# Optimization experiments

Measured on AMD Instinct MI355X. Metric: run time of the kernel, lower is better.

Reference implementation:

```python
import math
import jax, jax.numpy as jnp
import numpy as np

EMBED = 1024
HIDDEN = 1024
HEADS = 16


def setup_inputs() -> dict:
    key = jax.random.key(0)
    ks = jax.random.split(key, 9)
    B, S = 1, 4096
    s = 1.0 / math.sqrt(EMBED)
    return {
        "x": jax.random.normal(ks[0], (B, S, EMBED), dtype=jnp.float32),
        "Wq": jax.random.normal(ks[1], (EMBED, HIDDEN), dtype=jnp.float32) * s,
        "bq": jnp.zeros((HIDDEN,), dtype=jnp.float32),
        "Wk": jax.random.normal(ks[2], (EMBED, HIDDEN), dtype=jnp.float32) * s,
        "bk": jnp.zeros((HIDDEN,), dtype=jnp.float32),
        "Wv": jax.random.normal(ks[3], (EMBED, HIDDEN), dtype=jnp.float32) * s,
        "bv": jnp.zeros((HIDDEN,), dtype=jnp.float32),
        "Wo": jax.random.normal(ks[4], (EMBED, HIDDEN), dtype=jnp.float32) * s,
        "bo": jnp.zeros((HIDDEN,), dtype=jnp.float32),
    }


def reference(x, Wq, bq, Wk, bk, Wv, bv, Wo, bo):
    B, S, _ = x.shape
    Hd = HIDDEN // HEADS
    # projections: [B,S,hidden] -> [B,H,S,hd]
    def split_heads(t):
        return t.reshape(B, S, HEADS, Hd).transpose(0, 2, 1, 3)
    q = split_heads(x @ Wq + bq)
    k = split_heads(x @ Wk + bk)
    v = split_heads(x @ Wv + bv)
    scale = 1.0 / math.sqrt(EMBED / HEADS)
    scores = jnp.einsum("bhqd,bhkd->bhqk", q, k) * scale  # [B,H,S,S]
    attn = jax.nn.softmax(scores, axis=-1)
    ctx = jnp.einsum("bhqk,bhkd->bhqd", attn, v)
    ctx = ctx.transpose(0, 2, 1, 3).reshape(B, S, HIDDEN)
    return ctx @ Wo + bo
```

## Files before the change

### kernel.cpp

```cpp
#include <hip/hip_runtime.h>
#include <hip/hip_bf16.h>
#include <math.h>

typedef __bf16 bf16;
typedef bf16  bf16x2 __attribute__((ext_vector_type(2)));
typedef bf16  bf16x4 __attribute__((ext_vector_type(4)));
typedef bf16  bf16x8 __attribute__((ext_vector_type(8)));
typedef float f32x4  __attribute__((ext_vector_type(4)));
typedef float f32x16 __attribute__((ext_vector_type(16)));
typedef unsigned uint4v __attribute__((ext_vector_type(4)));

#define MFMA16(a, b, c) __builtin_amdgcn_mfma_f32_16x16x32_bf16((a), (b), (c), 0, 0, 0)
#define MFMA32(a, b, c) __builtin_amdgcn_mfma_f32_32x32x16_bf16((a), (b), (c), 0, 0, 0)

static constexpr int S  = 4096;
static constexpr int E  = 1024;
static constexpr int NH = 16;
static constexpr int HD = 64;

__device__ __forceinline__ void gload16(const bf16* g, bf16* l) {
    __builtin_amdgcn_global_load_lds(
        (const __attribute__((address_space(1))) void*)g,
        (__attribute__((address_space(3))) void*)l, 16, 0, 0);
}

__global__ void convert_f32_bf16(const float* __restrict__ in, bf16* __restrict__ out, int n) {
    int i = (blockIdx.x * blockDim.x + threadIdx.x) * 8;
    if (i < n) {
        float4 v0 = *(const float4*)(in + i);
        float4 v1 = *(const float4*)(in + i + 4);
        bf16x8 o = { (bf16)v0.x, (bf16)v0.y, (bf16)v0.z, (bf16)v0.w,
                     (bf16)v1.x, (bf16)v1.y, (bf16)v1.z, (bf16)v1.w };
        *(bf16x8*)(out + i) = o;
    }
}

__global__ void transpose_w(const float* __restrict__ W0, const float* __restrict__ W1,
                            const float* __restrict__ W2, const float* __restrict__ W3,
                            bf16* __restrict__ T0, bf16* __restrict__ T1,
                            bf16* __restrict__ T2, bf16* __restrict__ T3) {
    const float* W; bf16* T;
    switch (blockIdx.z) {
        case 0: W = W0; T = T0; break;
        case 1: W = W1; T = T1; break;
        case 2: W = W2; T = T2; break;
        default: W = W3; T = T3; break;
    }
    __shared__ float tile[64][65];
    int k0 = blockIdx.x * 64, n0 = blockIdx.y * 64;
    #pragma unroll
    for (int i = 0; i < 16; i++) {
        int idx = threadIdx.x + i * 256;
        int r = idx >> 6, c = idx & 63;
        tile[r][c] = W[(k0 + r) * E + n0 + c];
    }
    __syncthreads();
    #pragma unroll
    for (int i = 0; i < 8; i++) {
        int idx = threadIdx.x + i * 256;
        int r = idx >> 5, c2 = (idx & 31) * 2;
        bf16x2 v = { (bf16)tile[c2][r], (bf16)tile[c2 + 1][r] };
        *(bf16x2*)(T + (n0 + r) * E + k0 + c2) = v;
    }
}

template<int MODE>
__global__ __launch_bounds__(256) void gemm128(const bf16* __restrict__ A,
                                               const bf16* __restrict__ BT,
                                               const float* __restrict__ b0,
                                               const float* __restrict__ b1,
                                               const float* __restrict__ b2,
                                               void* __restrict__ out0,
                                               void* __restrict__ out1,
                                               void* __restrict__ out2,
                                               float qscale) {
    __shared__ __align__(16) bf16 Als[128 * 32];
    __shared__ __align__(16) bf16 Bls[128 * 32];
    const int tid = threadIdx.x, lane = tid & 63, w = tid >> 6;
    const int wm = w >> 1, wn = w & 1;
    const int m0 = blockIdx.x * 128, n0 = blockIdx.y * 128;
    const int ln = lane & 15, g = lane >> 4;

    const bf16* Ag = A  + (size_t)(m0 + w * 32 + (lane >> 2)) * E + (lane & 3) * 8;
    const bf16* Bg = BT + (size_t)(n0 + w * 32 + (lane >> 2)) * E + (lane & 3) * 8;

    f32x4 acc[4][4] = {};
    for (int kt = 0; kt < E; kt += 32) {
        __syncthreads();
        #pragma unroll
        for (int j = 0; j < 2; j++) {
            gload16(Ag + j * 16 * E + kt, (bf16*)((char*)Als + w * 2048 + j * 1024));
            gload16(Bg + j * 16 * E + kt, (bf16*)((char*)Bls + w * 2048 + j * 1024));
        }
        __syncthreads();
        bf16x8 af[4], bfr[4];
        #pragma unroll
        for (int i = 0; i < 4; i++) {
            af[i]  = *(const bf16x8*)(Als + (wm * 64 + i * 16 + ln) * 32 + g * 8);
            bfr[i] = *(const bf16x8*)(Bls + (wn * 64 + i * 16 + ln) * 32 + g * 8);
        }
        #pragma unroll
        for (int mi = 0; mi < 4; mi++)
            #pragma unroll
            for (int bj = 0; bj < 4; bj++)
                acc[mi][bj] = MFMA16(af[mi], bfr[bj], acc[mi][bj]);
    }

    if (MODE == 0) {
        const int proj = n0 >> 10;
        const float* bias = proj == 0 ? b0 : (proj == 1 ? b1 : b2);
        bf16* outp = (bf16*)(proj == 0 ? out0 : (proj == 1 ? out1 : out2));
        const float osc = proj == 0 ? qscale : 1.0f;
        if (proj < 2) {
            #pragma unroll
            for (int bj = 0; bj < 4; bj++) {
                const int n = n0 + wn * 64 + bj * 16 + ln;
                const int nn = n & 1023, hh = nn >> 6, dd = nn & 63;
                const float bb = bias[nn];
                #pragma unroll
                for (int mi = 0; mi < 4; mi++) {
                    const int m = m0 + wm * 64 + mi * 16 + g * 4;
                    #pragma unroll
                    for (int r = 0; r < 4; r++)
                        outp[((size_t)hh * S + m + r) * HD + dd] = (bf16)((acc[mi][bj][r] + bb) * osc);
                }
            }
        } else {
            #pragma unroll
            for (int bj = 0; bj < 4; bj++) {
                const int n = n0 + wn * 64 + bj * 16 + ln;
                const int nn = n & 1023;
                const float bb = bias[nn];
                #pragma unroll
                for (int mi = 0; mi < 4; mi++) {
                    const int m = m0 + wm * 64 + mi * 16 + g * 4;
                    bf16x4 vv = { (bf16)(acc[mi][bj][0] + bb), (bf16)(acc[mi][bj][1] + bb),
                                  (bf16)(acc[mi][bj][2] + bb), (bf16)(acc[mi][bj][3] + bb) };
                    *(bf16x4*)(outp + (size_t)nn * S + m) = vv;
                }
            }
        }
    } else {
        float* outp = (float*)out0;
        #pragma unroll
        for (int bj = 0; bj < 4; bj++) {
            const int n = n0 + wn * 64 + bj * 16 + ln;
            const float bb = b0[n];
            #pragma unroll
            for (int mi = 0; mi < 4; mi++) {
                const int m = m0 + wm * 64 + mi * 16 + g * 4;
                #pragma unroll
                for (int r = 0; r < 4; r++)
                    outp[(size_t)(m + r) * E + n] = acc[mi][bj][r] + bb;
            }
        }
    }
}

__global__ __launch_bounds__(512) void flash_attn5(const bf16* __restrict__ Qh,
                                                   const bf16* __restrict__ Kh,
                                                   const bf16* __restrict__ Vt,
                                                   bf16* __restrict__ ctx) {
    __shared__ __align__(16) char smem[65536];
    const int tid = threadIdx.x, lane = tid & 63, w = tid >> 6;
    const int w4 = w & 3, kvh = w >> 2;
    const int h = blockIdx.y, qb = blockIdx.x;
    const int l31 = lane & 31, h5 = lane >> 5;
    const int q_global = qb * 128 + w4 * 32 + l31;

    const bf16* Qbase = Qh + ((size_t)h * S + q_global) * HD;
    bf16x8 qf[4];
    #pragma unroll
    for (int t = 0; t < 4; t++) qf[t] = *(const bf16x8*)(Qbase + t * 16 + h5 * 8);

    const int srow = w4 * 16 + (lane >> 3);
    const int scol = ((lane & 7) ^ (lane >> 3)) * 8;
    const int swz  = (lane & 7) << 4;

    char* const Kb0 = smem + kvh * 16384;
    char* const Vb0 = smem + 32768 + kvh * 16384;

    auto stage = [&](int buf, int kv) {
        #pragma unroll
        for (int j = 0; j < 2; j++) {
            gload16(Kh + ((size_t)h * S + kv + srow + j * 8) * HD + scol,
                    (bf16*)(Kb0 + buf * 8192 + w4 * 2048 + j * 1024));
            gload16(Vt + ((size_t)(h * HD + srow + j * 8)) * S + kv + scol,
                    (bf16*)(Vb0 + buf * 8192 + w4 * 2048 + j * 1024));
        }
    };

    f32x16 o0 = {}, o1 = {};
    float l_i = 0.f;
    const int kv0 = kvh * (S / 2);
    constexpr int NT = S / 128;

    stage(0, kv0);
    for (int t = 0; t < NT; t++) {
        const int cur = t & 1;
        __syncthreads();
        if (t + 1 < NT) stage(cur ^ 1, kv0 + (t + 1) * 64);

        const char* Kb = Kb0 + cur * 8192;
        const char* Vb = Vb0 + cur * 8192;

        f32x16 s0 = {}, s1 = {};
        __builtin_amdgcn_s_setprio(1);
        #pragma unroll
        for (int t4 = 0; t4 < 4; t4++) {
            const int cb = (t4 * 32 + h5 * 16) ^ swz;
            bf16x8 k0 = *(const bf16x8*)(Kb + l31 * 128 + cb);
            bf16x8 k1 = *(const bf16x8*)(Kb + (32 + l31) * 128 + cb);
            s0 = MFMA32(k0, qf[t4], s0);
            s1 = MFMA32(k1, qf[t4], s1);
        }
        __builtin_amdgcn_s_setprio(0);

        bf16x8 pb[4];
        float rs = 0.f;
        {
            unsigned d[8];
            #pragma unroll
            for (int i = 0; i < 8; i++) {
                float e0 = __builtin_amdgcn_exp2f(s0[2 * i]);
                float e1 = __builtin_amdgcn_exp2f(s0[2 * i + 1]);
                rs += e0 + e1;
                asm("v_cvt_pk_bf16_f32 %0, %1, %2" : "=v"(d[i]) : "v"(e0), "v"(e1));
            }
            asm volatile("v_permlane32_swap_b32 %0, %1" : "+v"(d[0]), "+v"(d[2]));
            asm volatile("v_permlane32_swap_b32 %0, %1" : "+v"(d[1]), "+v"(d[3]));
            asm volatile("v_permlane32_swap_b32 %0, %1" : "+v"(d[4]), "+v"(d[6]));
            asm volatile("v_permlane32_swap_b32 %0, %1" : "+v"(d[5]), "+v"(d[7]));
            uint4v fa = { d[0], d[1], d[2], d[3] }, fb = { d[4], d[5], d[6], d[7] };
            pb[0] = __builtin_bit_cast(bf16x8, fa);
            pb[1] = __builtin_bit_cast(bf16x8, fb);
        }
        {
            unsigned d[8];
            #pragma unroll
            for (int i = 0; i < 8; i++) {
                float e0 = __builtin_amdgcn_exp2f(s1[2 * i]);
                float e1 = __builtin_amdgcn_exp2f(s1[2 * i + 1]);
                rs += e0 + e1;
                asm("v_cvt_pk_bf16_f32 %0, %1, %2" : "=v"(d[i]) : "v"(e0), "v"(e1));
            }
            asm volatile("v_permlane32_swap_b32 %0, %1" : "+v"(d[0]), "+v"(d[2]));
            asm volatile("v_permlane32_swap_b32 %0, %1" : "+v"(d[1]), "+v"(d[3]));
            asm volatile("v_permlane32_swap_b32 %0, %1" : "+v"(d[4]), "+v"(d[6]));
            asm volatile("v_permlane32_swap_b32 %0, %1" : "+v"(d[5]), "+v"(d[7]));
            uint4v fa = { d[0], d[1], d[2], d[3] }, fb = { d[4], d[5], d[6], d[7] };
            pb[2] = __builtin_bit_cast(bf16x8, fa);
            pb[3] = __builtin_bit_cast(bf16x8, fb);
        }
        l_i += rs;

        __builtin_amdgcn_s_setprio(1);
        #pragma unroll
        for (int ks = 0; ks < 4; ks++) {
            const int cb = (ks * 32 + h5 * 16) ^ swz;
            bf16x8 va  = *(const bf16x8*)(Vb + l31 * 128 + cb);
            bf16x8 vb2 = *(const bf16x8*)(Vb + (32 + l31) * 128 + cb);
            o0 = MFMA32(va, pb[ks], o0);
            o1 = MFMA32(vb2, pb[ks], o1);
        }
        __builtin_amdgcn_s_setprio(0);
    }

    __syncthreads();
    float* const lr  = (float*)(smem + 32768);
    float* const orr = (float*)smem + w4 * 2048;
    if (w >= 4) {
        lr[w4 * 64 + lane] = l_i;
        #pragma unroll
        for (int r = 0; r < 16; r++) orr[r * 64 + lane]        = o0[r];
        #pragma unroll
        for (int r = 0; r < 16; r++) orr[(16 + r) * 64 + lane] = o1[r];
    }
    __syncthreads();
    if (w < 4) {
        l_i += lr[w4 * 64 + lane];
        #pragma unroll
        for (int r = 0; r < 16; r++) o0[r] += orr[r * 64 + lane];
        #pragma unroll
        for (int r = 0; r < 16; r++) o1[r] += orr[(16 + r) * 64 + lane];
        l_i += __shfl_xor(l_i, 32);
        const float inv = 1.f / l_i;
        bf16* cbase = ctx + (size_t)q_global * E + h * HD;
        #pragma unroll
        for (int dg = 0; dg < 2; dg++) {
            const f32x16& o = dg ? o1 : o0;
            #pragma unroll
            for (int rq = 0; rq < 4; rq++) {
                bf16x4 ov = { (bf16)(o[rq * 4 + 0] * inv), (bf16)(o[rq * 4 + 1] * inv),
                              (bf16)(o[rq * 4 + 2] * inv), (bf16)(o[rq * 4 + 3] * inv) };
                *(bf16x4*)(cbase + dg * 32 + rq * 8 + h5 * 4) = ov;
            }
        }
    }
}

extern "C" void kernel_launch(void* const* d_in, const int* in_sizes, int n_in,
                              void* d_out, int out_size, void* d_ws, size_t ws_size,
                              hipStream_t stream) {
    const float* x  = (const float*)d_in[0];
    const float* Wq = (const float*)d_in[1];
    const float* bq = (const float*)d_in[2];
    const float* Wk = (const float*)d_in[3];
    const float* bk = (const float*)d_in[4];
    const float* Wv = (const float*)d_in[5];
    const float* bv = (const float*)d_in[6];
    const float* Wo = (const float*)d_in[7];
    const float* bo = (const float*)d_in[8];

    char* ws = (char*)d_ws;
    const size_t MB = 1u << 20;
    bf16* xb   = (bf16*)(ws + 0 * MB);
    bf16* Wcat = (bf16*)(ws + 8 * MB);
    bf16* tq   = Wcat;
    bf16* tk   = Wcat + 1024 * 1024;
    bf16* tv   = Wcat + 2048 * 1024;
    bf16* to   = (bf16*)(ws + 14 * MB);
    bf16* Qh   = (bf16*)(ws + 16 * MB);
    bf16* Kh   = (bf16*)(ws + 24 * MB);
    bf16* Vt   = (bf16*)(ws + 32 * MB);
    bf16* ctx  = (bf16*)(ws + 40 * MB);

    const float qscale = 0.125f * 1.44269504088896f;

    convert_f32_bf16<<<dim3(S * E / 2048), 256, 0, stream>>>(x, xb, S * E);
    transpose_w<<<dim3(16, 16, 4), 256, 0, stream>>>(Wq, Wk, Wv, Wo, tq, tk, tv, to);

    gemm128<0><<<dim3(S / 128, 3072 / 128), 256, 0, stream>>>(
        xb, Wcat, bq, bk, bv, Qh, Kh, Vt, qscale);

    flash_attn5<<<dim3(S / 128, NH), 512, 0, stream>>>(Qh, Kh, Vt, ctx);

    gemm128<1><<<dim3(S / 128, E / 128), 256, 0, stream>>>(
        ctx, to, bo, nullptr, nullptr, d_out, nullptr, nullptr, 1.0f);
}
```

Before: 154.4 us.

## Software-pipeline flash attention so P·V of prior tile overlaps next QK^T

Restructures the attention loop so the P·V MFMAs for the previous KV tile are interleaved with the QK^T MFMAs for the current tile, with the exp/pack step moved after both. V gets a triple buffer (K stays double buffered), which grows dynamic LDS from 64 KB to 80 KB, and launch bounds now request 4 waves per SIMD. The goal is to hide exp/convert latency behind matrix work and keep the MFMA pipe busy. The costs are more LDS per block, which may limit occupancy, and extra prologue and epilogue code.

```diff
diff --git a/kernel.cpp b/kernel.cpp
--- a/kernel.cpp
+++ b/kernel.cpp
@@ -157,11 +157,11 @@
     }
 }
 
-__global__ __launch_bounds__(512) void flash_attn5(const bf16* __restrict__ Qh,
-                                                   const bf16* __restrict__ Kh,
-                                                   const bf16* __restrict__ Vt,
-                                                   bf16* __restrict__ ctx) {
-    __shared__ __align__(16) char smem[65536];
+__global__ __launch_bounds__(512, 4) void flash_attn6(const bf16* __restrict__ Qh,
+                                                      const bf16* __restrict__ Kh,
+                                                      const bf16* __restrict__ Vt,
+                                                      bf16* __restrict__ ctx) {
+    extern __shared__ char smem[];
     const int tid = threadIdx.x, lane = tid & 63, w = tid >> 6;
     const int w4 = w & 3, kvh = w >> 2;
     const int h = blockIdx.y, qb = blockIdx.x;
@@ -178,15 +178,15 @@
     const int swz  = (lane & 7) << 4;
 
     char* const Kb0 = smem + kvh * 16384;
-    char* const Vb0 = smem + 32768 + kvh * 16384;
-
-    auto stage = [&](int buf, int kv) {
+    char* const Vb0 = smem + 32768 + kvh * 24576;
+
+    auto stage = [&](int kb, int vb, int kv) {
         #pragma unroll
         for (int j = 0; j < 2; j++) {
             gload16(Kh + ((size_t)h * S + kv + srow + j * 8) * HD + scol,
-                    (bf16*)(Kb0 + buf * 8192 + w4 * 2048 + j * 1024));
+                    (bf16*)(Kb0 + kb * 8192 + w4 * 2048 + j * 1024));
             gload16(Vt + ((size_t)(h * HD + srow + j * 8)) * S + kv + scol,
-                    (bf16*)(Vb0 + buf * 8192 + w4 * 2048 + j * 1024));
+                    (bf16*)(Vb0 + vb * 8192 + w4 * 2048 + j * 1024));
         }
     };
 
@@ -195,74 +195,87 @@
     const int kv0 = kvh * (S / 2);
     constexpr int NT = S / 128;
 
-    stage(0, kv0);
-    for (int t = 0; t < NT; t++) {
-        const int cur = t & 1;
+    bf16x8 pbP[4];
+
+    auto qks = [&](const char* Kb, int rowoff, f32x16& s) {
+        #pragma unroll
+        for (int t4 = 0; t4 < 4; t4++) {
+            const int cb = (t4 * 32 + h5 * 16) ^ swz;
+            bf16x8 kk = *(const bf16x8*)(Kb + (rowoff + l31) * 128 + cb);
+            s = MFMA32(kk, qf[t4], s);
+        }
+    };
+    auto pvpair = [&](const char* Vp, int kscol, const bf16x8& p) {
+        const int cb = (kscol + h5 * 16) ^ swz;
+        bf16x8 va  = *(const bf16x8*)(Vp + l31 * 128 + cb);
+        bf16x8 vb2 = *(const bf16x8*)(Vp + (32 + l31) * 128 + cb);
+        o0 = MFMA32(va, p, o0);
+        o1 = MFMA32(vb2, p, o1);
+    };
+    auto exppack = [&](const f32x16& s, bf16x8& pa, bf16x8& pc, float& rs) {
+        unsigned d[8];
+        #pragma unroll
+        for (int i = 0; i < 8; i++) {
+            float e0 = __builtin_amdgcn_exp2f(s[2 * i]);
+            float e1 = __builtin_amdgcn_exp2f(s[2 * i + 1]);
+            rs += e0 + e1;
+            asm("v_cvt_pk_bf16_f32 %0, %1, %2" : "=v"(d[i]) : "v"(e0), "v"(e1));
+        }
+        asm volatile("v_permlane32_swap_b32 %0, %1" : "+v"(d[0]), "+v"(d[2]));
+        asm volatile("v_permlane32_swap_b32 %0, %1" : "+v"(d[1]), "+v"(d[3]));
+        asm volatile("v_permlane32_swap_b32 %0, %1" : "+v"(d[4]), "+v"(d[6]));
+        asm volatile("v_permlane32_swap_b32 %0, %1" : "+v"(d[5]), "+v"(d[7]));
+        uint4v fa = { d[0], d[1], d[2], d[3] }, fb = { d[4], d[5], d[6], d[7] };
+        pa = __builtin_bit_cast(bf16x8, fa);
+        pc = __builtin_bit_cast(bf16x8, fb);
+    };
+
+    stage(0, 0, kv0);
+
+    {
         __syncthreads();
-        if (t + 1 < NT) stage(cur ^ 1, kv0 + (t + 1) * 64);
-
-        const char* Kb = Kb0 + cur * 8192;
-        const char* Vb = Vb0 + cur * 8192;
-
+        stage(1, 1, kv0 + 64);
+        const char* Kb = Kb0;
         f32x16 s0 = {}, s1 = {};
         __builtin_amdgcn_s_setprio(1);
-        #pragma unroll
-        for (int t4 = 0; t4 < 4; t4++) {
-            const int cb = (t4 * 32 + h5 * 16) ^ swz;
-            bf16x8 k0 = *(const bf16x8*)(Kb + l31 * 128 + cb);
-            bf16x8 k1 = *(const bf16x8*)(Kb + (32 + l31) * 128 + cb);
-            s0 = MFMA32(k0, qf[t4], s0);
-            s1 = MFMA32(k1, qf[t4], s1);
-        }
+        qks(Kb, 0, s0);
+        qks(Kb, 32, s1);
         __builtin_amdgcn_s_setprio(0);
-
-        bf16x8 pb[4];
         float rs = 0.f;
-        {
-            unsigned d[8];
-            #pragma unroll
-            for (int i = 0; i < 8; i++) {
-                float e0 = __builtin_amdgcn_exp2f(s0[2 * i]);
-                float e1 = __builtin_amdgcn_exp2f(s0[2 * i + 1]);
-                rs += e0 + e1;
-                asm("v_cvt_pk_bf16_f32 %0, %1, %2" : "=v"(d[i]) : "v"(e0), "v"(e1));
-            }
-            asm volatile("v_permlane32_swap_b32 %0, %1" : "+v"(d[0]), "+v"(d[2]));
-            asm volatile("v_permlane32_swap_b32 %0, %1" : "+v"(d[1]), "+v"(d[3]));
-            asm volatile("v_permlane32_swap_b32 %0, %1" : "+v"(d[4]), "+v"(d[6]));
-            asm volatile("v_permlane32_swap_b32 %0, %1" : "+v"(d[5]), "+v"(d[7]));
-            uint4v fa = { d[0], d[1], d[2], d[3] }, fb = { d[4], d[5], d[6], d[7] };
-            pb[0] = __builtin_bit_cast(bf16x8, fa);
-            pb[1] = __builtin_bit_cast(bf16x8, fb);
-        }
-        {
-            unsigned d[8];
-            #pragma unroll
-            for (int i = 0; i < 8; i++) {
-                float e0 = __builtin_amdgcn_exp2f(s1[2 * i]);
-                float e1 = __builtin_amdgcn_exp2f(s1[2 * i + 1]);
-                rs += e0 + e1;
-                asm("v_cvt_pk_bf16_f32 %0, %1, %2" : "=v"(d[i]) : "v"(e0), "v"(e1));
-            }
-            asm volatile("v_permlane32_swap_b32 %0, %1" : "+v"(d[0]), "+v"(d[2]));
-            asm volatile("v_permlane32_swap_b32 %0, %1" : "+v"(d[1]), "+v"(d[3]));
-            asm volatile("v_permlane32_swap_b32 %0, %1" : "+v"(d[4]), "+v"(d[6]));
-            asm volatile("v_permlane32_swap_b32 %0, %1" : "+v"(d[5]), "+v"(d[7]));
-            uint4v fa = { d[0], d[1], d[2], d[3] }, fb = { d[4], d[5], d[6], d[7] };
-            pb[2] = __builtin_bit_cast(bf16x8, fa);
-            pb[3] = __builtin_bit_cast(bf16x8, fb);
-        }
+        exppack(s0, pbP[0], pbP[1], rs);
+        exppack(s1, pbP[2], pbP[3], rs);
         l_i += rs;
-
+    }
+
+    for (int t = 1; t < NT; t++) {
+        __syncthreads();
+        if (t + 1 < NT) stage((t + 1) & 1, (t + 1) % 3, kv0 + (t + 1) * 64);
+        const char* Kb = Kb0 + (t & 1) * 8192;
+        const char* Vp = Vb0 + ((t - 1) % 3) * 8192;
+
+        f32x16 s0 = {}, s1 = {};
         __builtin_amdgcn_s_setprio(1);
-        #pragma unroll
-        for (int ks = 0; ks < 4; ks++) {
-            const int cb = (ks * 32 + h5 * 16) ^ swz;
-            bf16x8 va  = *(const bf16x8*)(Vb + l31 * 128 + cb);
-            bf16x8 vb2 = *(const bf16x8*)(Vb + (32 + l31) * 128 + cb);
-            o0 = MFMA32(va, pb[ks], o0);
-            o1 = MFMA32(vb2, pb[ks], o1);
-        }
+        qks(Kb, 0, s0);
+        pvpair(Vp, 0,  pbP[0]);
+        pvpair(Vp, 32, pbP[1]);
+        qks(Kb, 32, s1);
+        pvpair(Vp, 64, pbP[2]);
+        pvpair(Vp, 96, pbP[3]);
+        __builtin_amdgcn_s_setprio(0);
+
+        float rs = 0.f;
+        exppack(s0, pbP[0], pbP[1], rs);
+        exppack(s1, pbP[2], pbP[3], rs);
+        l_i += rs;
+    }
+
+    {
+        const char* Vp = Vb0 + ((NT - 1) % 3) * 8192;
+        __builtin_amdgcn_s_setprio(1);
+        pvpair(Vp, 0,  pbP[0]);
+        pvpair(Vp, 32, pbP[1]);
+        pvpair(Vp, 64, pbP[2]);
+        pvpair(Vp, 96, pbP[3]);
         __builtin_amdgcn_s_setprio(0);
     }
 
@@ -333,7 +346,7 @@
     gemm128<0><<<dim3(S / 128, 3072 / 128), 256, 0, stream>>>(
         xb, Wcat, bq, bk, bv, Qh, Kh, Vt, qscale);
 
-    flash_attn5<<<dim3(S / 128, NH), 512, 0, stream>>>(Qh, Kh, Vt, ctx);
+    flash_attn6<<<dim3(S / 128, NH), 512, 81920, stream>>>(Qh, Kh, Vt, ctx);
 
     gemm128<1><<<dim3(S / 128, E / 128), 256, 0, stream>>>(
         ctx, to, bo, nullptr, nullptr, d_out, nullptr, nullptr, 1.0f);
```

After: 156.2 us. No clear change (+1.2%).

## Give each attention warp two query tiles and split KV into four quarters

Applied to the files above, without the earlier changes.

The flash-attention kernel now has each warp process 64 queries as two 32-row tiles. Each K and V fragment read from LDS feeds two MFMAs instead of one, roughly halving LDS read traffic per MFMA. The KV range is split four ways across warp pairs instead of two, with the partial outputs reduced through shared memory at the end. In exchange, the block uses 128 KB of dynamic LDS and holds more accumulator registers per thread, which can reduce occupancy and risks register spills under the launch bound.

```diff
diff --git a/kernel.cpp b/kernel.cpp
--- a/kernel.cpp
+++ b/kernel.cpp
@@ -157,143 +157,158 @@
     }
 }
 
-__global__ __launch_bounds__(512) void flash_attn5(const bf16* __restrict__ Qh,
-                                                   const bf16* __restrict__ Kh,
-                                                   const bf16* __restrict__ Vt,
-                                                   bf16* __restrict__ ctx) {
-    __shared__ __align__(16) char smem[65536];
+__global__ __launch_bounds__(512, 2) void flash_attn7(const bf16* __restrict__ Qh,
+                                                      const bf16* __restrict__ Kh,
+                                                      const bf16* __restrict__ Vt,
+                                                      bf16* __restrict__ ctx) {
+    extern __shared__ char smem[];
     const int tid = threadIdx.x, lane = tid & 63, w = tid >> 6;
-    const int w4 = w & 3, kvh = w >> 2;
+    const int qsub = w & 1, quarter = w >> 1;
     const int h = blockIdx.y, qb = blockIdx.x;
     const int l31 = lane & 31, h5 = lane >> 5;
-    const int q_global = qb * 128 + w4 * 32 + l31;
-
-    const bf16* Qbase = Qh + ((size_t)h * S + q_global) * HD;
-    bf16x8 qf[4];
+
+    const bf16* Qb0 = Qh + ((size_t)h * S + qb * 128 + qsub * 64 + l31) * HD;
+    bf16x8 qf0[4], qf1[4];
     #pragma unroll
-    for (int t = 0; t < 4; t++) qf[t] = *(const bf16x8*)(Qbase + t * 16 + h5 * 8);
-
-    const int srow = w4 * 16 + (lane >> 3);
+    for (int t = 0; t < 4; t++) {
+        qf0[t] = *(const bf16x8*)(Qb0 + t * 16 + h5 * 8);
+        qf1[t] = *(const bf16x8*)(Qb0 + 32 * HD + t * 16 + h5 * 8);
+    }
+
+    const int srow = qsub * 32 + (lane >> 3);
     const int scol = ((lane & 7) ^ (lane >> 3)) * 8;
     const int swz  = (lane & 7) << 4;
 
-    char* const Kb0 = smem + kvh * 16384;
-    char* const Vb0 = smem + 32768 + kvh * 16384;
+    char* const Kq = smem + quarter * 16384;
+    char* const Vq = smem + 65536 + quarter * 16384;
 
     auto stage = [&](int buf, int kv) {
         #pragma unroll
-        for (int j = 0; j < 2; j++) {
+        for (int j = 0; j < 4; j++) {
             gload16(Kh + ((size_t)h * S + kv + srow + j * 8) * HD + scol,
-                    (bf16*)(Kb0 + buf * 8192 + w4 * 2048 + j * 1024));
+                    (bf16*)(Kq + buf * 8192 + qsub * 4096 + j * 1024));
             gload16(Vt + ((size_t)(h * HD + srow + j * 8)) * S + kv + scol,
-                    (bf16*)(Vb0 + buf * 8192 + w4 * 2048 + j * 1024));
+                    (bf16*)(Vq + buf * 8192 + qsub * 4096 + j * 1024));
         }
     };
 
-    f32x16 o0 = {}, o1 = {};
-    float l_i = 0.f;
-    const int kv0 = kvh * (S / 2);
-    constexpr int NT = S / 128;
+    auto exppack = [&](const f32x16& s, bf16x8& pa, bf16x8& pc, float& rs) {
+        unsigned d[8];
+        #pragma unroll
+        for (int i = 0; i < 8; i++) {
+            float e0 = __builtin_amdgcn_exp2f(s[2 * i]);
+            float e1 = __builtin_amdgcn_exp2f(s[2 * i + 1]);
+            rs += e0 + e1;
+            asm("v_cvt_pk_bf16_f32 %0, %1, %2" : "=v"(d[i]) : "v"(e0), "v"(e1));
+        }
+        asm volatile("v_permlane32_swap_b32 %0, %1" : "+v"(d[0]), "+v"(d[2]));
+        asm volatile("v_permlane32_swap_b32 %0, %1" : "+v"(d[1]), "+v"(d[3]));
+        asm volatile("v_permlane32_swap_b32 %0, %1" : "+v"(d[4]), "+v"(d[6]));
+        asm volatile("v_permlane32_swap_b32 %0, %1" : "+v"(d[5]), "+v"(d[7]));
+        uint4v fa = { d[0], d[1], d[2], d[3] }, fb = { d[4], d[5], d[6], d[7] };
+        pa = __builtin_bit_cast(bf16x8, fa);
+        pc = __builtin_bit_cast(bf16x8, fb);
+    };
+
+    f32x16 o00 = {}, o01 = {}, o10 = {}, o11 = {};
+    float l0 = 0.f, l1 = 0.f;
+    const int kv0 = quarter * (S / 4);
+    constexpr int NT = S / 256;
 
     stage(0, kv0);
     for (int t = 0; t < NT; t++) {
         const int cur = t & 1;
         __syncthreads();
         if (t + 1 < NT) stage(cur ^ 1, kv0 + (t + 1) * 64);
-
-        const char* Kb = Kb0 + cur * 8192;
-        const char* Vb = Vb0 + cur * 8192;
-
-        f32x16 s0 = {}, s1 = {};
-        __builtin_amdgcn_s_setprio(1);
-        #pragma unroll
-        for (int t4 = 0; t4 < 4; t4++) {
-            const int cb = (t4 * 32 + h5 * 16) ^ swz;
-            bf16x8 k0 = *(const bf16x8*)(Kb + l31 * 128 + cb);
-            bf16x8 k1 = *(const bf16x8*)(Kb + (32 + l31) * 128 + cb);
-            s0 = MFMA32(k0, qf[t4], s0);
-            s1 = MFMA32(k1, qf[t4], s1);
-        }
-        __builtin_amdgcn_s_setprio(0);
-
-        bf16x8 pb[4];
-        float rs = 0.f;
-        {
-            unsigned d[8];
-            #pragma unroll
-            for (int i = 0; i < 8; i++) {
-                float e0 = __builtin_amdgcn_exp2f(s0[2 * i]);
-                float e1 = __builtin_amdgcn_exp2f(s0[2 * i + 1]);
-                rs += e0 + e1;
-                asm("v_cvt_pk_bf16_f32 %0, %1, %2" : "=v"(d[i]) : "v"(e0), "v"(e1));
-            }
-            asm volatile("v_permlane32_swap_b32 %0, %1" : "+v"(d[0]), "+v"(d[2]));
-            asm volatile("v_permlane32_swap_b32 %0, %1" : "+v"(d[1]), "+v"(d[3]));
-            asm volatile("v_permlane32_swap_b32 %0, %1" : "+v"(d[4]), "+v"(d[6]));
-            asm volatile("v_permlane32_swap_b32 %0, %1" : "+v"(d[5]), "+v"(d[7]));
-            uint4v fa = { d[0], d[1], d[2], d[3] }, fb = { d[4], d[5], d[6], d[7] };
-            pb[0] = __builtin_bit_cast(bf16x8, fa);
-            pb[1] = __builtin_bit_cast(bf16x8, fb);
-        }
-        {
-            unsigned d[8];
-            #pragma unroll
-            for (int i = 0; i < 8; i++) {
-                float e0 = __builtin_amdgcn_exp2f(s1[2 * i]);
-                float e1 = __builtin_amdgcn_exp2f(s1[2 * i + 1]);
-                rs += e0 + e1;
-                asm("v_cvt_pk_bf16_f32 %0, %1, %2" : "=v"(d[i]) : "v"(e0), "v"(e1));
-            }
-            asm volatile("v_permlane32_swap_b32 %0, %1" : "+v"(d[0]), "+v"(d[2]));
-            asm volatile("v_permlane32_swap_b32 %0, %1" : "+v"(d[1]), "+v"(d[3]));
-            asm volatile("v_permlane32_swap_b32 %0, %1" : "+v"(d[4]), "+v"(d[6]));
-            asm volatile("v_permlane32_swap_b32 %0, %1" : "+v"(d[5]), "+v"(d[7]));
-            uint4v fa = { d[0], d[1], d[2], d[3] }, fb = { d[4], d[5], d[6], d[7] };
-            pb[2] = __builtin_bit_cast(bf16x8, fa);
-            pb[3] = __builtin_bit_cast(bf16x8, fb);
-        }
-        l_i += rs;
-
-        __builtin_amdgcn_s_setprio(1);
-        #pragma unroll
-        for (int ks = 0; ks < 4; ks++) {
-            const int cb = (ks * 32 + h5 * 16) ^ swz;
-            bf16x8 va  = *(const bf16x8*)(Vb + l31 * 128 + cb);
-            bf16x8 vb2 = *(const bf16x8*)(Vb + (32 + l31) * 128 + cb);
-            o0 = MFMA32(va, pb[ks], o0);
-            o1 = MFMA32(vb2, pb[ks], o1);
-        }
-        __builtin_amdgcn_s_setprio(0);
+        const char* Kb = Kq + cur * 8192;
+        const char* Vb = Vq + cur * 8192;
+
+        #pragma unroll
+        for (int khalf = 0; khalf < 2; khalf++) {
+            f32x16 s0 = {}, s1 = {};
+            __builtin_amdgcn_s_setprio(1);
+            #pragma unroll
+            for (int t4 = 0; t4 < 4; t4++) {
+                const int cb = (t4 * 32 + h5 * 16) ^ swz;
+                bf16x8 kk = *(const bf16x8*)(Kb + (khalf * 32 + l31) * 128 + cb);
+                s0 = MFMA32(kk, qf0[t4], s0);
+                s1 = MFMA32(kk, qf1[t4], s1);
+            }
+            __builtin_amdgcn_s_setprio(0);
+
+            bf16x8 p00, p01, p10, p11;
+            exppack(s0, p00, p01, l0);
+            exppack(s1, p10, p11, l1);
+
+            __builtin_amdgcn_s_setprio(1);
+            #pragma unroll
+            for (int sub = 0; sub < 2; sub++) {
+                const int cbv = ((khalf * 2 + sub) * 32 + h5 * 16) ^ swz;
+                const bf16x8 pA = sub ? p01 : p00;
+                const bf16x8 pB = sub ? p11 : p10;
+                bf16x8 va0 = *(const bf16x8*)(Vb + l31 * 128 + cbv);
+                bf16x8 va1 = *(const bf16x8*)(Vb + (32 + l31) * 128 + cbv);
+                o00 = MFMA32(va0, pA, o00);
+                o01 = MFMA32(va0, pB, o01);
+                o10 = MFMA32(va1, pA, o10);
+                o11 = MFMA32(va1, pB, o11);
+            }
+            __builtin_amdgcn_s_setprio(0);
+        }
     }
 
     __syncthreads();
-    float* const lr  = (float*)(smem + 32768);
-    float* const orr = (float*)smem + w4 * 2048;
-    if (w >= 4) {
-        lr[w4 * 64 + lane] = l_i;
-        #pragma unroll
-        for (int r = 0; r < 16; r++) orr[r * 64 + lane]        = o0[r];
-        #pragma unroll
-        for (int r = 0; r < 16; r++) orr[(16 + r) * 64 + lane] = o1[r];
+    float* const Ob = (float*)smem;
+    float* const Lb = (float*)(smem + 98304);
+    if (quarter != 0) {
+        const int reg = qsub * 3 + (quarter - 1);
+        float* Or = Ob + reg * 4096;
+        #pragma unroll
+        for (int r = 0; r < 16; r++) Or[r * 64 + lane]          = o00[r];
+        #pragma unroll
+        for (int r = 0; r < 16; r++) Or[(16 + r) * 64 + lane]   = o01[r];
+        #pragma unroll
+        for (int r = 0; r < 16; r++) Or[(32 + r) * 64 + lane]   = o10[r];
+        #pragma unroll
+        for (int r = 0; r < 16; r++) Or[(48 + r) * 64 + lane]   = o11[r];
+        Lb[reg * 128 + lane]      = l0;
+        Lb[reg * 128 + 64 + lane] = l1;
     }
     __syncthreads();
-    if (w < 4) {
-        l_i += lr[w4 * 64 + lane];
-        #pragma unroll
-        for (int r = 0; r < 16; r++) o0[r] += orr[r * 64 + lane];
-        #pragma unroll
-        for (int r = 0; r < 16; r++) o1[r] += orr[(16 + r) * 64 + lane];
-        l_i += __shfl_xor(l_i, 32);
-        const float inv = 1.f / l_i;
-        bf16* cbase = ctx + (size_t)q_global * E + h * HD;
+    if (quarter == 0) {
+        #pragma unroll
+        for (int p = 0; p < 3; p++) {
+            const int reg = qsub * 3 + p;
+            float* Or = Ob + reg * 4096;
+            #pragma unroll
+            for (int r = 0; r < 16; r++) o00[r] += Or[r * 64 + lane];
+            #pragma unroll
+            for (int r = 0; r < 16; r++) o01[r] += Or[(16 + r) * 64 + lane];
+            #pragma unroll
+            for (int r = 0; r < 16; r++) o10[r] += Or[(32 + r) * 64 + lane];
+            #pragma unroll
+            for (int r = 0; r < 16; r++) o11[r] += Or[(48 + r) * 64 + lane];
+            l0 += Lb[reg * 128 + lane];
+            l1 += Lb[reg * 128 + 64 + lane];
+        }
+        l0 += __shfl_xor(l0, 32);
+        l1 += __shfl_xor(l1, 32);
+        const float inv0 = 1.f / l0, inv1 = 1.f / l1;
+
+        bf16* c0 = ctx + (size_t)(qb * 128 + qsub * 64 + l31) * E + h * HD;
+        bf16* c1 = c0 + (size_t)32 * E;
         #pragma unroll
         for (int dg = 0; dg < 2; dg++) {
-            const f32x16& o = dg ? o1 : o0;
+            const f32x16& oa = dg ? o10 : o00;
+            const f32x16& ob = dg ? o11 : o01;
             #pragma unroll
             for (int rq = 0; rq < 4; rq++) {
-                bf16x4 ov = { (bf16)(o[rq * 4 + 0] * inv), (bf16)(o[rq * 4 + 1] * inv),
-                              (bf16)(o[rq * 4 + 2] * inv), (bf16)(o[rq * 4 + 3] * inv) };
-                *(bf16x4*)(cbase + dg * 32 + rq * 8 + h5 * 4) = ov;
+                bf16x4 va = { (bf16)(oa[rq * 4 + 0] * inv0), (bf16)(oa[rq * 4 + 1] * inv0),
+                              (bf16)(oa[rq * 4 + 2] * inv0), (bf16)(oa[rq * 4 + 3] * inv0) };
+                bf16x4 vb = { (bf16)(ob[rq * 4 + 0] * inv1), (bf16)(ob[rq * 4 + 1] * inv1),
+                              (bf16)(ob[rq * 4 + 2] * inv1), (bf16)(ob[rq * 4 + 3] * inv1) };
+                *(bf16x4*)(c0 + dg * 32 + rq * 8 + h5 * 4) = va;
+                *(bf16x4*)(c1 + dg * 32 + rq * 8 + h5 * 4) = vb;
             }
         }
     }
@@ -333,7 +348,7 @@
     gemm128<0><<<dim3(S / 128, 3072 / 128), 256, 0, stream>>>(
         xb, Wcat, bq, bk, bv, Qh, Kh, Vt, qscale);
 
-    flash_attn5<<<dim3(S / 128, NH), 512, 0, stream>>>(Qh, Kh, Vt, ctx);
+    flash_attn7<<<dim3(S / 128, NH), 512, 131072, stream>>>(Qh, Kh, Vt, ctx);
 
     gemm128<1><<<dim3(S / 128, E / 128), 256, 0, stream>>>(
         ctx, to, bo, nullptr, nullptr, d_out, nullptr, nullptr, 1.0f);
```

After: 161.4 us. 4.5% more time.
